# Optimization experiments

Measured on AMD Instinct MI355X. Metric: run time of the kernel, lower is better.

## Reference

```python
import jax, jax.numpy as jnp
import numpy as np

N = 50000      # nodes
E = 800000     # edges
F = 128        # input features
H = 128        # hidden dim
G = 1024       # graphs in batch
EPS = 1e-5


def setup_inputs() -> dict:
    key = jax.random.key(0)
    ks = jax.random.split(key, 16)
    s = 0.05
    return {
        "x": jax.random.normal(ks[0], (N, F), dtype=jnp.float32),
        "edge_index": jax.random.randint(ks[1], (2, E), 0, N, dtype=jnp.int64),
        "batch": jnp.sort(jax.random.randint(ks[2], (N,), 0, G, dtype=jnp.int64)),
        "convW0": jax.random.normal(ks[3], (F, H), dtype=jnp.float32) * s,
        "convW": jax.random.normal(ks[4], (2, H, H), dtype=jnp.float32) * s,  # layers 1,2
        "convb": jax.random.normal(ks[5], (3, H), dtype=jnp.float32) * s,
        "bn_gamma": jnp.ones((3, H), dtype=jnp.float32),
        "bn_beta": jnp.zeros((3, H), dtype=jnp.float32),
        "mW1": jax.random.normal(ks[6], (2 * H, 256), dtype=jnp.float32) * s,
        "mb1": jnp.zeros((256,), dtype=jnp.float32),
        "mW2": jax.random.normal(ks[7], (256, 128), dtype=jnp.float32) * s,
        "mb2": jnp.zeros((128,), dtype=jnp.float32),
        "mW3": jax.random.normal(ks[8], (128, 1), dtype=jnp.float32) * s,
        "mb3": jnp.zeros((1,), dtype=jnp.float32),
    }


def _gcn_norm(edge_index):
    # add self-loops, compute sym-normalization coeffs (PyG GCNConv default)
    loop = jnp.arange(N, dtype=edge_index.dtype)
    src = jnp.concatenate([edge_index[0], loop])
    dst = jnp.concatenate([edge_index[1], loop])
    deg = jax.ops.segment_sum(jnp.ones_like(dst, dtype=jnp.float32), dst, num_segments=N)
    dinv = jax.lax.rsqrt(deg)  # deg >= 1 due to self loops
    norm = dinv[src] * dinv[dst]  # [E+N]
    return src, dst, norm


def _gcn_layer(x, W, b, src, dst, norm):
    h = x @ W                               # [N, H]
    msg = h[src] * norm[:, None]            # gather + scale, [E+N, H]
    agg = jax.ops.segment_sum(msg, dst, num_segments=N)
    return agg + b


def _batchnorm(x, gamma, beta):
    mu = jnp.mean(x, axis=0)
    var = jnp.mean(jnp.square(x - mu), axis=0)  # biased, as torch training fwd
    return gamma * (x - mu) * jax.lax.rsqrt(var + EPS) + beta


def reference(x, edge_index, batch, convW0, convW, convb, bn_gamma, bn_beta,
              mW1, mb1, mW2, mb2, mW3, mb3):
    src, dst, norm = _gcn_norm(edge_index)
    Ws = [convW0, convW[0], convW[1]]
    for i in range(3):
        x = _gcn_layer(x, Ws[i], convb[i], src, dst, norm)
        x = _batchnorm(x, bn_gamma[i], bn_beta[i])
        x = jax.nn.relu(x)
        # dropout: identity in eval mode
    ones = jnp.ones((N,), dtype=x.dtype)
    counts = jax.ops.segment_sum(ones, batch, num_segments=G)  # [G]
    x_mean = jax.ops.segment_sum(x, batch, num_segments=G) / jnp.maximum(counts, 1.0)[:, None]
    x_max = jax.ops.segment_max(x, batch, num_segments=G)
    x_max = jnp.where(counts[:, None] > 0, x_max, 0.0)
    g = jnp.concatenate([x_mean, x_max], axis=1)  # [G, 2H]
    h = jax.nn.relu(g @ mW1 + mb1)
    h = jax.nn.relu(h @ mW2 + mb2)
    out = h @ mW3 + mb3                            # [G, 1]
    return out.squeeze(1)
```

## Files before the change

kernel.cpp:

```cpp
#include <hip/hip_runtime.h>


constexpr int FH = 128;
constexpr int GG = 1024;
constexpr int NSB = 256;
constexpr int BKS = 1024;
constexpr int CPAD = 16;
constexpr int EPB = 4096;
constexpr float EPSV = 1e-5f;

typedef __attribute__((ext_vector_type(8))) short short8v;
typedef __attribute__((ext_vector_type(4))) float f32x4;

__device__ inline unsigned short bf16_rn(float x) {
    unsigned u = __float_as_uint(x);
    unsigned r = (u + 0x7FFFu + ((u >> 16) & 1u)) >> 16;
    return (unsigned short)r;
}
__device__ inline float bflo(unsigned u) { return __uint_as_float(u << 16); }
__device__ inline float bfhi(unsigned u) { return __uint_as_float(u & 0xFFFF0000u); }
__device__ inline float4 bf4tof(ushort4 h) {
    return make_float4(__uint_as_float((unsigned)h.x << 16),
                       __uint_as_float((unsigned)h.y << 16),
                       __uint_as_float((unsigned)h.z << 16),
                       __uint_as_float((unsigned)h.w << 16));
}

__global__ void k_deg(const int* __restrict__ dst, unsigned* __restrict__ deg, int E) {
    int e = blockIdx.x * 256 + threadIdx.x;
    if (e < E) atomicAdd(&deg[dst[e]], 1u);
}

__global__ void k_dinv(const unsigned* __restrict__ deg, float* __restrict__ dinv, int n) {
    int i = blockIdx.x * 256 + threadIdx.x;
    if (i < n) dinv[i] = rsqrtf((float)deg[i] + 1.0f);
}

__global__ __launch_bounds__(1024) void k_scan1(const unsigned* __restrict__ deg,
                                                int* __restrict__ rowptr, int* __restrict__ bsum, int n) {
    __shared__ int wsum[16];
    int i = blockIdx.x * 1024 + threadIdx.x;
    int lane = threadIdx.x & 63, wid = threadIdx.x >> 6;
    int v = (i < n) ? (int)deg[i] : 0;
    int incl = v;
    #pragma unroll
    for (int off = 1; off < 64; off <<= 1) {
        int t = __shfl_up(incl, off, 64);
        if (lane >= off) incl += t;
    }
    if (lane == 63) wsum[wid] = incl;
    __syncthreads();
    int woff = 0;
    #pragma unroll
    for (int w = 0; w < 16; ++w) woff += (w < wid) ? wsum[w] : 0;
    if (i < n) rowptr[i] = woff + incl - v;
    if (threadIdx.x == 1023) bsum[blockIdx.x] = woff + incl;
}

__global__ void k_scan2(int* __restrict__ bsum, int* __restrict__ rowptr_n, int nb) {
    int lane = threadIdx.x;
    int v = (lane < nb) ? bsum[lane] : 0;
    int incl = v;
    #pragma unroll
    for (int off = 1; off < 64; off <<= 1) {
        int t = __shfl_up(incl, off, 64);
        if (lane >= off) incl += t;
    }
    if (lane < nb) bsum[lane] = incl - v;
    if (lane == 63) *rowptr_n = incl;
}

__global__ __launch_bounds__(1024) void k_scan3(int* __restrict__ rowptr,
                                                const int* __restrict__ bsum, int n) {
    int i = blockIdx.x * 1024 + threadIdx.x;
    if (i < n) rowptr[i] += bsum[blockIdx.x];
}

__global__ void k_bcur(const int* __restrict__ rowptr, int* __restrict__ bcur, int nbk) {
    int k = blockIdx.x * 256 + threadIdx.x;
    if (k < nbk) bcur[k * CPAD] = rowptr[k << 6];
}

__global__ __launch_bounds__(256) void k_binscatter(const int* __restrict__ src, const int* __restrict__ dst,
                                                    int* __restrict__ bcur, uint2* __restrict__ tmp,
                                                    int E, int nbk) {
    __shared__ int hist[BKS];
    int tid = threadIdx.x;
    for (int b = tid; b < nbk; b += 256) hist[b] = 0;
    __syncthreads();
    int e0 = blockIdx.x * EPB;
    int s[16], d[16];
    #pragma unroll
    for (int i = 0; i < 16; ++i) {
        int e = e0 + i * 256 + tid;
        if (e < E) {
            s[i] = src[e]; d[i] = dst[e];
            atomicAdd(&hist[d[i] >> 6], 1);
        } else d[i] = -1;
    }
    __syncthreads();
    for (int b = tid; b < nbk; b += 256) {
        int c = hist[b];
        hist[b] = c ? atomicAdd(&bcur[b * CPAD], c) : 0;
    }
    __syncthreads();
    #pragma unroll
    for (int i = 0; i < 16; ++i) {
        if (d[i] >= 0) {
            int p = atomicAdd(&hist[d[i] >> 6], 1);
            tmp[p] = make_uint2((unsigned)s[i], (unsigned)d[i]);
        }
    }
}

__global__ __launch_bounds__(256) void k_finesort(const uint2* __restrict__ tmp,
                                                  const int* __restrict__ rowptr,
                                                  int* __restrict__ csr_src, int n) {
    __shared__ int cur[64];
    int nb0 = blockIdx.x << 6;
    int tid = threadIdx.x;
    int hi = min(nb0 + 64, n);
    if (tid < 64 && nb0 + tid < n) cur[tid] = rowptr[nb0 + tid];
    __syncthreads();
    int estart = rowptr[nb0], eend = rowptr[hi];
    for (int e = estart + tid; e < eend; e += 256) {
        uint2 pr = tmp[e];
        int p = atomicAdd(&cur[pr.y & 63], 1);
        csr_src[p] = (int)pr.x;
    }
}

__global__ void k_gptr(const int* __restrict__ batch, int* __restrict__ gptr, int n) {
    int g = blockIdx.x * 256 + threadIdx.x;
    if (g > GG) return;
    int lo = 0, hi = n;
    while (lo < hi) { int mid = (lo + hi) >> 1; if (batch[mid] < g) lo = mid + 1; else hi = mid; }
    gptr[g] = lo;
}

__global__ void k_wprep(const float* __restrict__ W0, const float* __restrict__ W12,
                        unsigned short* __restrict__ Wt) {
    int t = blockIdx.x * 256 + threadIdx.x;
    int l = t >> 14, o = t & 16383;
    const float* W = (l == 0) ? W0 : W12 + (size_t)(l - 1) * 16384;
    int j = o & 7, c = (o >> 3) & 15, hi = (o >> 7) & 3, kb = (o >> 9) & 3, nt = o >> 11;
    int k = kb * 32 + hi * 8 + j;
    int col = nt * 16 + c;
    Wt[t] = bf16_rn(W[k * 128 + col]);
}

template<bool BF16IN>
__global__ __launch_bounds__(256) void k_gemm(const void* __restrict__ Xp,
                                              const unsigned short* __restrict__ Wt,
                                              const float* __restrict__ dinv,
                                              const float* __restrict__ sc,
                                              const float* __restrict__ sh,
                                              unsigned short* __restrict__ H, int n) {
    int wave = threadIdx.x >> 6, L = threadIdx.x & 63;
    int hi = L >> 4, c16 = L & 15;
    int m0 = blockIdx.x * 64 + wave * 16;
    int arow = m0 + c16;
    bool okA = arow < n;

    short8v aF[4];
    #pragma unroll
    for (int kb = 0; kb < 4; ++kb) {
        int kc = kb * 32 + hi * 8;
        float v[8];
        #pragma unroll
        for (int j = 0; j < 8; ++j) v[j] = 0.f;
        if (okA) {
            if constexpr (BF16IN) {
                const unsigned short* Xb = (const unsigned short*)Xp;
                uint4 raw = *(const uint4*)&Xb[(size_t)arow * 128 + kc];
                v[0] = bflo(raw.x); v[1] = bfhi(raw.x);
                v[2] = bflo(raw.y); v[3] = bfhi(raw.y);
                v[4] = bflo(raw.z); v[5] = bfhi(raw.z);
                v[6] = bflo(raw.w); v[7] = bfhi(raw.w);
                float4 s0 = *(const float4*)&sc[kc], s1 = *(const float4*)&sc[kc + 4];
                float4 h0 = *(const float4*)&sh[kc], h1 = *(const float4*)&sh[kc + 4];
                v[0] = fmaxf(fmaf(v[0], s0.x, h0.x), 0.f);
                v[1] = fmaxf(fmaf(v[1], s0.y, h0.y), 0.f);
                v[2] = fmaxf(fmaf(v[2], s0.z, h0.z), 0.f);
                v[3] = fmaxf(fmaf(v[3], s0.w, h0.w), 0.f);
                v[4] = fmaxf(fmaf(v[4], s1.x, h1.x), 0.f);
                v[5] = fmaxf(fmaf(v[5], s1.y, h1.y), 0.f);
                v[6] = fmaxf(fmaf(v[6], s1.z, h1.z), 0.f);
                v[7] = fmaxf(fmaf(v[7], s1.w, h1.w), 0.f);
            } else {
                const float* Xf = (const float*)Xp;
                float4 v0 = *(const float4*)&Xf[(size_t)arow * 128 + kc];
                float4 v1 = *(const float4*)&Xf[(size_t)arow * 128 + kc + 4];
                v[0] = v0.x; v[1] = v0.y; v[2] = v0.z; v[3] = v0.w;
                v[4] = v1.x; v[5] = v1.y; v[6] = v1.z; v[7] = v1.w;
            }
        }
        short8v a;
        #pragma unroll
        for (int j = 0; j < 8; ++j) a[j] = (short)bf16_rn(v[j]);
        aF[kb] = a;
    }

    f32x4 acc[8];
    #pragma unroll
    for (int nt = 0; nt < 8; ++nt) {
        acc[nt][0] = 0.f; acc[nt][1] = 0.f; acc[nt][2] = 0.f; acc[nt][3] = 0.f;
    }
    #pragma unroll
    for (int nt = 0; nt < 8; ++nt) {
        #pragma unroll
        for (int kb = 0; kb < 4; ++kb) {
            short8v bF = *(const short8v*)&Wt[(size_t)(nt * 4 + kb) * 512 + L * 8];
            acc[nt] = __builtin_amdgcn_mfma_f32_16x16x32_bf16(aF[kb], bF, acc[nt], 0, 0, 0);
        }
    }

    #pragma unroll
    for (int reg = 0; reg < 4; ++reg) {
        int row = m0 + hi * 4 + reg;
        if (row < n) {
            float dv = dinv[row];
            #pragma unroll
            for (int nt = 0; nt < 8; ++nt)
                H[(size_t)row * 128 + nt * 16 + c16] = bf16_rn(acc[nt][reg] * dv);
        }
    }
}

__global__ __launch_bounds__(256) void k_aggregate(const int* __restrict__ rowptr, const int* __restrict__ csr_src,
                                                   const float* __restrict__ dinv,
                                                   const unsigned short* __restrict__ H2,
                                                   unsigned short* __restrict__ Bo, int n) {
    int node = blockIdx.x * 8 + (threadIdx.x >> 5);
    if (node >= n) return;
    int lane = threadIdx.x & 31;
    int beg = rowptr[node], end = rowptr[node + 1];
    float dv = dinv[node];
    const ushort4* Hv = (const ushort4*)H2;
    float4 acc = bf4tof(Hv[(size_t)node * 32 + lane]);
    float4 acc2 = make_float4(0.f, 0.f, 0.f, 0.f);
    int e = beg;
    for (; e + 1 < end; e += 2) {
        int s0 = csr_src[e], s1 = csr_src[e + 1];
        float4 h0 = bf4tof(Hv[(size_t)s0 * 32 + lane]);
        float4 h1 = bf4tof(Hv[(size_t)s1 * 32 + lane]);
        acc.x += h0.x;  acc.y += h0.y;  acc.z += h0.z;  acc.w += h0.w;
        acc2.x += h1.x; acc2.y += h1.y; acc2.z += h1.z; acc2.w += h1.w;
    }
    if (e < end) {
        int s0 = csr_src[e];
        float4 h0 = bf4tof(Hv[(size_t)s0 * 32 + lane]);
        acc.x += h0.x; acc.y += h0.y; acc.z += h0.z; acc.w += h0.w;
    }
    ushort4 o;
    o.x = bf16_rn((acc.x + acc2.x) * dv);
    o.y = bf16_rn((acc.y + acc2.y) * dv);
    o.z = bf16_rn((acc.z + acc2.z) * dv);
    o.w = bf16_rn((acc.w + acc2.w) * dv);
    *(ushort4*)&Bo[(size_t)node * 128 + lane * 4] = o;
}

__global__ __launch_bounds__(256) void k_stats(const unsigned short* __restrict__ X,
                                               float* __restrict__ partials, int n) {
    __shared__ float sb[4][128];
    int tid = threadIdx.x;
    int fp = tid & 63, sub = tid >> 6;
    float s0 = 0.f, s1 = 0.f, q0 = 0.f, q1 = 0.f;
    for (int r = blockIdx.x * 4 + sub; r < n; r += NSB * 4) {
        unsigned u = *(const unsigned*)&X[(size_t)r * 128 + fp * 2];
        float v0 = bflo(u), v1 = bfhi(u);
        s0 += v0; q0 = fmaf(v0, v0, q0);
        s1 += v1; q1 = fmaf(v1, v1, q1);
    }
    sb[sub][fp * 2] = s0; sb[sub][fp * 2 + 1] = s1;
    __syncthreads();
    if (tid < 128) partials[(size_t)blockIdx.x * 256 + tid] =
        sb[0][tid] + sb[1][tid] + sb[2][tid] + sb[3][tid];
    __syncthreads();
    sb[sub][fp * 2] = q0; sb[sub][fp * 2 + 1] = q1;
    __syncthreads();
    if (tid < 128) partials[(size_t)blockIdx.x * 256 + 128 + tid] =
        sb[0][tid] + sb[1][tid] + sb[2][tid] + sb[3][tid];
}

__global__ __launch_bounds__(128) void k_finstats(const float* __restrict__ partials,
                                                  const float* __restrict__ gamma, const float* __restrict__ beta,
                                                  float* __restrict__ sc, float* __restrict__ sh, int n) {
    int f = threadIdx.x;
    float s = 0.f, q = 0.f;
    for (int b = 0; b < NSB; ++b) {
        s += partials[(size_t)b * 256 + f];
        q += partials[(size_t)b * 256 + 128 + f];
    }
    float invN = 1.0f / (float)n;
    float mu = s * invN;
    float var = fmaf(-mu, mu, q * invN);
    float scale = gamma[f] * rsqrtf(var + EPSV);
    sc[f] = scale;
    sh[f] = fmaf(-mu, scale, beta[f]);
}

__global__ __launch_bounds__(256) void k_pool(const unsigned short* __restrict__ X, const int* __restrict__ gptr,
                                              const float* __restrict__ sc, const float* __restrict__ sh,
                                              float* __restrict__ pooled) {
    __shared__ float shm[256];
    int g = blockIdx.x;
    int t = threadIdx.x;
    int f = t & 127, sub = t >> 7;
    int beg = gptr[g], end = gptr[g + 1];
    float scf = sc[f], shf = sh[f];
    float s = 0.f, m = 0.f;
    for (int r = beg + sub; r < end; r += 2) {
        float xv = __uint_as_float((unsigned)X[(size_t)r * 128 + f] << 16);
        float v = fmaxf(fmaf(xv, scf, shf), 0.f);
        s += v; m = fmaxf(m, v);
    }
    shm[t] = s;
    __syncthreads();
    if (sub == 0) {
        int c = end - beg;
        float inv = (c > 0) ? 1.0f / (float)c : 0.f;
        pooled[(size_t)g * 256 + f] = (s + shm[t + 128]) * inv;
    }
    __syncthreads();
    shm[t] = m;
    __syncthreads();
    if (sub == 1) {
        pooled[(size_t)g * 256 + 128 + f] = fmaxf(m, shm[t - 128]);
    }
}

__global__ __launch_bounds__(256) void k_mlp1(const float* __restrict__ pooled, const float* __restrict__ W1,
                                              const float* __restrict__ b1, float* __restrict__ H1) {
    __shared__ float grow[256];
    int gi = blockIdx.x, t = threadIdx.x;
    grow[t] = pooled[(size_t)gi * 256 + t];
    __syncthreads();
    float acc = b1[t];
    #pragma unroll 8
    for (int k = 0; k < 256; ++k) acc = fmaf(grow[k], W1[k * 256 + t], acc);
    H1[gi * 256 + t] = fmaxf(acc, 0.f);
}

__global__ __launch_bounds__(128) void k_mlp2(const float* __restrict__ H1, const float* __restrict__ W2,
                                              const float* __restrict__ b2, float* __restrict__ H2) {
    __shared__ float row[256];
    int gi = blockIdx.x, t = threadIdx.x;
    row[t] = H1[gi * 256 + t];
    row[t + 128] = H1[gi * 256 + t + 128];
    __syncthreads();
    float acc = b2[t];
    #pragma unroll 8
    for (int k = 0; k < 256; ++k) acc = fmaf(row[k], W2[k * 128 + t], acc);
    H2[gi * 128 + t] = fmaxf(acc, 0.f);
}

__global__ __launch_bounds__(256) void k_mlp3(const float* __restrict__ H2, const float* __restrict__ W3,
                                              const float* __restrict__ b3, float* __restrict__ out) {
    int gi = blockIdx.x * 4 + (threadIdx.x >> 6);
    int lane = threadIdx.x & 63;
    float v = H2[gi * 128 + lane] * W3[lane] + H2[gi * 128 + 64 + lane] * W3[64 + lane];
    #pragma unroll
    for (int off = 32; off; off >>= 1) v += __shfl_down(v, off);
    if (lane == 0) out[gi] = v + b3[0];
}

extern "C" void kernel_launch(void* const* d_in, const int* in_sizes, int n_in,
                              void* d_out, int out_size, void* d_ws, size_t ws_size,
                              hipStream_t stream) {
    const float* x      = (const float*)d_in[0];
    const int*   ei     = (const int*)d_in[1];
    const int*   batch  = (const int*)d_in[2];
    const float* convW0 = (const float*)d_in[3];
    const float* convW  = (const float*)d_in[4];
    const float* gamma  = (const float*)d_in[6];
    const float* beta   = (const float*)d_in[7];
    const float* mW1    = (const float*)d_in[8];
    const float* mb1    = (const float*)d_in[9];
    const float* mW2    = (const float*)d_in[10];
    const float* mb2    = (const float*)d_in[11];
    const float* mW3    = (const float*)d_in[12];
    const float* mb3    = (const float*)d_in[13];
    float* out = (float*)d_out;

    const int E = in_sizes[1] / 2;
    const int n = in_sizes[0] / FH;
    const int npad = (n + 4) & ~3;
    const int nb = (n + 1023) / 1024;
    const int nbk = (n + 63) >> 6;

    float*          A     = (float*)d_ws;
    unsigned short* H2b   = (unsigned short*)A;
    uint2*          tmp   = (uint2*)A;
    float*    B       = A + (size_t)n * FH;
    unsigned short* Bb = (unsigned short*)B;
    int*      bcur    = (int*)B;
    float*    dinv    = B + (size_t)n * FH;
    unsigned* deg     = (unsigned*)(dinv + n);
    float*    parts   = (float*)(deg + n);
    float*    sc      = parts + (size_t)NSB * 256;
    float*    sh      = sc + 128;
    float*    pooled  = sh + 128;
    float*    h1      = pooled + (size_t)GG * 256;
    float*    h2      = h1 + (size_t)GG * 256;
    int*      gptr    = (int*)(h2 + (size_t)GG * FH);
    int*      rowptr  = gptr + ((GG + 4) & ~3);
    int*      bsum    = rowptr + npad;
    int*      csrsrc  = bsum + 64;
    unsigned short* Wt = (unsigned short*)(csrsrc + ((E + 3) & ~3));

    const int* srcI = ei;
    const int* dstI = ei + E;

    hipMemsetAsync(deg, 0, (size_t)n * sizeof(unsigned), stream);
    k_deg<<<(E + 255) / 256, 256, 0, stream>>>(dstI, deg, E);
    k_dinv<<<(n + 255) / 256, 256, 0, stream>>>(deg, dinv, n);
    k_scan1<<<nb, 1024, 0, stream>>>(deg, rowptr, bsum, n);
    k_scan2<<<1, 64, 0, stream>>>(bsum, rowptr + n, nb);
    k_scan3<<<nb, 1024, 0, stream>>>(rowptr, bsum, n);
    k_bcur<<<(nbk + 255) / 256, 256, 0, stream>>>(rowptr, bcur, nbk);
    k_binscatter<<<(E + EPB - 1) / EPB, 256, 0, stream>>>(srcI, dstI, bcur, tmp, E, nbk);
    k_finesort<<<nbk, 256, 0, stream>>>(tmp, rowptr, csrsrc, n);
    k_gptr<<<(GG + 1 + 255) / 256, 256, 0, stream>>>(batch, gptr, n);
    k_wprep<<<3 * 16384 / 256, 256, 0, stream>>>(convW0, convW, Wt);

    for (int l = 0; l < 3; ++l) {
        if (l == 0)
            k_gemm<false><<<(n + 63) / 64, 256, 0, stream>>>(x, Wt, dinv, nullptr, nullptr, H2b, n);
        else
            k_gemm<true><<<(n + 63) / 64, 256, 0, stream>>>(Bb, Wt + (size_t)l * 16384, dinv, sc, sh, H2b, n);
        k_aggregate<<<(n + 7) / 8, 256, 0, stream>>>(rowptr, csrsrc, dinv, H2b, Bb, n);
        k_stats<<<NSB, 256, 0, stream>>>(Bb, parts, n);
        k_finstats<<<1, 128, 0, stream>>>(parts, gamma + l * FH, beta + l * FH, sc, sh, n);
    }

    k_pool<<<GG, 256, 0, stream>>>(Bb, gptr, sc, sh, pooled);
    k_mlp1<<<GG, 256, 0, stream>>>(pooled, mW1, mb1, h1);
    k_mlp2<<<GG, 128, 0, stream>>>(h1, mW2, mb2, h2);
    k_mlp3<<<GG / 4, 256, 0, stream>>>(h2, mW3, mb3, out);
}
```

Baseline: 421.8 us.

## Fuse setup and MLP kernels, widen aggregate loads, pack sort keys to 32 bits

Folds the dinv computation into scan1 and the bucket-cursor init into scan3, and merges mlp2 with mlp3 to cut launches and an intermediate buffer. The aggregation kernel now uses 16 lanes per node with 16-byte loads and 4-way unrolled gathers to raise memory-level parallelism. Sort temporaries are packed into a single 32-bit word, halving scatter traffic. This assumes node ids fit in 16 bits. BN statistics use fewer partial blocks, with a two-half reduction in finstats.

```diff
diff --git a/kernel.cpp b/kernel.cpp
--- a/kernel.cpp
+++ b/kernel.cpp
@@ -3,7 +3,7 @@
 
 constexpr int FH = 128;
 constexpr int GG = 1024;
-constexpr int NSB = 256;
+constexpr int NSB = 128;
 constexpr int BKS = 1024;
 constexpr int CPAD = 16;
 constexpr int EPB = 4096;
@@ -19,29 +19,20 @@
 }
 __device__ inline float bflo(unsigned u) { return __uint_as_float(u << 16); }
 __device__ inline float bfhi(unsigned u) { return __uint_as_float(u & 0xFFFF0000u); }
-__device__ inline float4 bf4tof(ushort4 h) {
-    return make_float4(__uint_as_float((unsigned)h.x << 16),
-                       __uint_as_float((unsigned)h.y << 16),
-                       __uint_as_float((unsigned)h.z << 16),
-                       __uint_as_float((unsigned)h.w << 16));
-}
 
 __global__ void k_deg(const int* __restrict__ dst, unsigned* __restrict__ deg, int E) {
     int e = blockIdx.x * 256 + threadIdx.x;
     if (e < E) atomicAdd(&deg[dst[e]], 1u);
 }
 
-__global__ void k_dinv(const unsigned* __restrict__ deg, float* __restrict__ dinv, int n) {
-    int i = blockIdx.x * 256 + threadIdx.x;
-    if (i < n) dinv[i] = rsqrtf((float)deg[i] + 1.0f);
-}
-
 __global__ __launch_bounds__(1024) void k_scan1(const unsigned* __restrict__ deg,
-                                                int* __restrict__ rowptr, int* __restrict__ bsum, int n) {
+                                                int* __restrict__ rowptr, int* __restrict__ bsum,
+                                                float* __restrict__ dinv, int n) {
     __shared__ int wsum[16];
     int i = blockIdx.x * 1024 + threadIdx.x;
     int lane = threadIdx.x & 63, wid = threadIdx.x >> 6;
     int v = (i < n) ? (int)deg[i] : 0;
+    if (i < n) dinv[i] = rsqrtf((float)v + 1.0f);
     int incl = v;
     #pragma unroll
     for (int off = 1; off < 64; off <<= 1) {
@@ -71,18 +62,18 @@
 }
 
 __global__ __launch_bounds__(1024) void k_scan3(int* __restrict__ rowptr,
-                                                const int* __restrict__ bsum, int n) {
+                                                const int* __restrict__ bsum,
+                                                int* __restrict__ bcur, int n) {
     int i = blockIdx.x * 1024 + threadIdx.x;
-    if (i < n) rowptr[i] += bsum[blockIdx.x];
-}
-
-__global__ void k_bcur(const int* __restrict__ rowptr, int* __restrict__ bcur, int nbk) {
-    int k = blockIdx.x * 256 + threadIdx.x;
-    if (k < nbk) bcur[k * CPAD] = rowptr[k << 6];
+    if (i < n) {
+        int r = rowptr[i] + bsum[blockIdx.x];
+        rowptr[i] = r;
+        if ((i & 63) == 0) bcur[(i >> 6) * CPAD] = r;
+    }
 }
 
 __global__ __launch_bounds__(256) void k_binscatter(const int* __restrict__ src, const int* __restrict__ dst,
-                                                    int* __restrict__ bcur, uint2* __restrict__ tmp,
+                                                    int* __restrict__ bcur, unsigned* __restrict__ tmp,
                                                     int E, int nbk) {
     __shared__ int hist[BKS];
     int tid = threadIdx.x;
@@ -108,12 +99,12 @@
     for (int i = 0; i < 16; ++i) {
         if (d[i] >= 0) {
             int p = atomicAdd(&hist[d[i] >> 6], 1);
-            tmp[p] = make_uint2((unsigned)s[i], (unsigned)d[i]);
+            tmp[p] = (unsigned)s[i] | ((unsigned)(d[i] & 63) << 16);
         }
     }
 }
 
-__global__ __launch_bounds__(256) void k_finesort(const uint2* __restrict__ tmp,
+__global__ __launch_bounds__(256) void k_finesort(const unsigned* __restrict__ tmp,
                                                   const int* __restrict__ rowptr,
                                                   int* __restrict__ csr_src, int n) {
     __shared__ int cur[64];
@@ -124,9 +115,9 @@
     __syncthreads();
     int estart = rowptr[nb0], eend = rowptr[hi];
     for (int e = estart + tid; e < eend; e += 256) {
-        uint2 pr = tmp[e];
-        int p = atomicAdd(&cur[pr.y & 63], 1);
-        csr_src[p] = (int)pr.x;
+        unsigned pr = tmp[e];
+        int p = atomicAdd(&cur[(pr >> 16) & 63], 1);
+        csr_src[p] = (int)(pr & 0xFFFFu);
     }
 }
 
@@ -231,33 +222,47 @@
                                                    const float* __restrict__ dinv,
                                                    const unsigned short* __restrict__ H2,
                                                    unsigned short* __restrict__ Bo, int n) {
-    int node = blockIdx.x * 8 + (threadIdx.x >> 5);
+    int node = blockIdx.x * 16 + (threadIdx.x >> 4);
     if (node >= n) return;
-    int lane = threadIdx.x & 31;
+    int lane = threadIdx.x & 15;
     int beg = rowptr[node], end = rowptr[node + 1];
     float dv = dinv[node];
-    const ushort4* Hv = (const ushort4*)H2;
-    float4 acc = bf4tof(Hv[(size_t)node * 32 + lane]);
-    float4 acc2 = make_float4(0.f, 0.f, 0.f, 0.f);
+    const uint4* Hv = (const uint4*)H2;
+    float a0[8], a1[8];
+    {
+        uint4 u = Hv[(size_t)node * 16 + lane];
+        a0[0] = bflo(u.x); a0[1] = bfhi(u.x); a0[2] = bflo(u.y); a0[3] = bfhi(u.y);
+        a0[4] = bflo(u.z); a0[5] = bfhi(u.z); a0[6] = bflo(u.w); a0[7] = bfhi(u.w);
+        #pragma unroll
+        for (int j = 0; j < 8; ++j) a1[j] = 0.f;
+    }
     int e = beg;
-    for (; e + 1 < end; e += 2) {
-        int s0 = csr_src[e], s1 = csr_src[e + 1];
-        float4 h0 = bf4tof(Hv[(size_t)s0 * 32 + lane]);
-        float4 h1 = bf4tof(Hv[(size_t)s1 * 32 + lane]);
-        acc.x += h0.x;  acc.y += h0.y;  acc.z += h0.z;  acc.w += h0.w;
-        acc2.x += h1.x; acc2.y += h1.y; acc2.z += h1.z; acc2.w += h1.w;
-    }
-    if (e < end) {
+    for (; e + 3 < end; e += 4) {
+        int s0 = csr_src[e], s1 = csr_src[e + 1], s2 = csr_src[e + 2], s3 = csr_src[e + 3];
+        uint4 u0 = Hv[(size_t)s0 * 16 + lane];
+        uint4 u1 = Hv[(size_t)s1 * 16 + lane];
+        uint4 u2 = Hv[(size_t)s2 * 16 + lane];
+        uint4 u3 = Hv[(size_t)s3 * 16 + lane];
+        a0[0] += bflo(u0.x); a0[1] += bfhi(u0.x); a0[2] += bflo(u0.y); a0[3] += bfhi(u0.y);
+        a0[4] += bflo(u0.z); a0[5] += bfhi(u0.z); a0[6] += bflo(u0.w); a0[7] += bfhi(u0.w);
+        a1[0] += bflo(u1.x); a1[1] += bfhi(u1.x); a1[2] += bflo(u1.y); a1[3] += bfhi(u1.y);
+        a1[4] += bflo(u1.z); a1[5] += bfhi(u1.z); a1[6] += bflo(u1.w); a1[7] += bfhi(u1.w);
+        a0[0] += bflo(u2.x); a0[1] += bfhi(u2.x); a0[2] += bflo(u2.y); a0[3] += bfhi(u2.y);
+        a0[4] += bflo(u2.z); a0[5] += bfhi(u2.z); a0[6] += bflo(u2.w); a0[7] += bfhi(u2.w);
+        a1[0] += bflo(u3.x); a1[1] += bfhi(u3.x); a1[2] += bflo(u3.y); a1[3] += bfhi(u3.y);
+        a1[4] += bflo(u3.z); a1[5] += bfhi(u3.z); a1[6] += bflo(u3.w); a1[7] += bfhi(u3.w);
+    }
+    for (; e < end; ++e) {
         int s0 = csr_src[e];
-        float4 h0 = bf4tof(Hv[(size_t)s0 * 32 + lane]);
-        acc.x += h0.x; acc.y += h0.y; acc.z += h0.z; acc.w += h0.w;
-    }
-    ushort4 o;
-    o.x = bf16_rn((acc.x + acc2.x) * dv);
-    o.y = bf16_rn((acc.y + acc2.y) * dv);
-    o.z = bf16_rn((acc.z + acc2.z) * dv);
-    o.w = bf16_rn((acc.w + acc2.w) * dv);
-    *(ushort4*)&Bo[(size_t)node * 128 + lane * 4] = o;
+        uint4 u0 = Hv[(size_t)s0 * 16 + lane];
+        a0[0] += bflo(u0.x); a0[1] += bfhi(u0.x); a0[2] += bflo(u0.y); a0[3] += bfhi(u0.y);
+        a0[4] += bflo(u0.z); a0[5] += bfhi(u0.z); a0[6] += bflo(u0.w); a0[7] += bfhi(u0.w);
+    }
+    unsigned w0 = (unsigned)bf16_rn((a0[0] + a1[0]) * dv) | ((unsigned)bf16_rn((a0[1] + a1[1]) * dv) << 16);
+    unsigned w1 = (unsigned)bf16_rn((a0[2] + a1[2]) * dv) | ((unsigned)bf16_rn((a0[3] + a1[3]) * dv) << 16);
+    unsigned w2 = (unsigned)bf16_rn((a0[4] + a1[4]) * dv) | ((unsigned)bf16_rn((a0[5] + a1[5]) * dv) << 16);
+    unsigned w3 = (unsigned)bf16_rn((a0[6] + a1[6]) * dv) | ((unsigned)bf16_rn((a0[7] + a1[7]) * dv) << 16);
+    ((uint4*)Bo)[(size_t)node * 16 + lane] = make_uint4(w0, w1, w2, w3);
 }
 
 __global__ __launch_bounds__(256) void k_stats(const unsigned short* __restrict__ X,
@@ -283,21 +288,32 @@
         sb[0][tid] + sb[1][tid] + sb[2][tid] + sb[3][tid];
 }
 
-__global__ __launch_bounds__(128) void k_finstats(const float* __restrict__ partials,
+__global__ __launch_bounds__(256) void k_finstats(const float* __restrict__ partials,
                                                   const float* __restrict__ gamma, const float* __restrict__ beta,
                                                   float* __restrict__ sc, float* __restrict__ sh, int n) {
-    int f = threadIdx.x;
+    __shared__ float red[256];
+    int t = threadIdx.x;
+    int f = t & 127, half = t >> 7;
     float s = 0.f, q = 0.f;
-    for (int b = 0; b < NSB; ++b) {
+    for (int b = half * (NSB / 2); b < (half + 1) * (NSB / 2); ++b) {
         s += partials[(size_t)b * 256 + f];
         q += partials[(size_t)b * 256 + 128 + f];
     }
-    float invN = 1.0f / (float)n;
-    float mu = s * invN;
-    float var = fmaf(-mu, mu, q * invN);
-    float scale = gamma[f] * rsqrtf(var + EPSV);
-    sc[f] = scale;
-    sh[f] = fmaf(-mu, scale, beta[f]);
+    red[t] = s;
+    __syncthreads();
+    float s_tot = red[f] + red[f + 128];
+    __syncthreads();
+    red[t] = q;
+    __syncthreads();
+    if (half == 0) {
+        float q_tot = red[f] + red[f + 128];
+        float invN = 1.0f / (float)n;
+        float mu = s_tot * invN;
+        float var = fmaf(-mu, mu, q_tot * invN);
+        float scale = gamma[f] * rsqrtf(var + EPSV);
+        sc[f] = scale;
+        sh[f] = fmaf(-mu, scale, beta[f]);
+    }
 }
 
 __global__ __launch_bounds__(256) void k_pool(const unsigned short* __restrict__ X, const int* __restrict__ gptr,
@@ -342,9 +358,11 @@
     H1[gi * 256 + t] = fmaxf(acc, 0.f);
 }
 
-__global__ __launch_bounds__(128) void k_mlp2(const float* __restrict__ H1, const float* __restrict__ W2,
-                                              const float* __restrict__ b2, float* __restrict__ H2) {
+__global__ __launch_bounds__(128) void k_mlp23(const float* __restrict__ H1, const float* __restrict__ W2,
+                                               const float* __restrict__ b2, const float* __restrict__ W3,
+                                               const float* __restrict__ b3, float* __restrict__ out) {
     __shared__ float row[256];
+    __shared__ float wred[2];
     int gi = blockIdx.x, t = threadIdx.x;
     row[t] = H1[gi * 256 + t];
     row[t + 128] = H1[gi * 256 + t + 128];
@@ -352,17 +370,12 @@
     float acc = b2[t];
     #pragma unroll 8
     for (int k = 0; k < 256; ++k) acc = fmaf(row[k], W2[k * 128 + t], acc);
-    H2[gi * 128 + t] = fmaxf(acc, 0.f);
-}
-
-__global__ __launch_bounds__(256) void k_mlp3(const float* __restrict__ H2, const float* __restrict__ W3,
-                                              const float* __restrict__ b3, float* __restrict__ out) {
-    int gi = blockIdx.x * 4 + (threadIdx.x >> 6);
-    int lane = threadIdx.x & 63;
-    float v = H2[gi * 128 + lane] * W3[lane] + H2[gi * 128 + 64 + lane] * W3[64 + lane];
+    float v = fmaxf(acc, 0.f) * W3[t];
     #pragma unroll
     for (int off = 32; off; off >>= 1) v += __shfl_down(v, off);
-    if (lane == 0) out[gi] = v + b3[0];
+    if ((t & 63) == 0) wred[t >> 6] = v;
+    __syncthreads();
+    if (t == 0) out[gi] = wred[0] + wred[1] + b3[0];
 }
 
 extern "C" void kernel_launch(void* const* d_in, const int* in_sizes, int n_in,
@@ -391,7 +404,7 @@
 
     float*          A     = (float*)d_ws;
     unsigned short* H2b   = (unsigned short*)A;
-    uint2*          tmp   = (uint2*)A;
+    unsigned*       tmp   = (unsigned*)A;
     float*    B       = A + (size_t)n * FH;
     unsigned short* Bb = (unsigned short*)B;
     int*      bcur    = (int*)B;
@@ -402,8 +415,7 @@
     float*    sh      = sc + 128;
     float*    pooled  = sh + 128;
     float*    h1      = pooled + (size_t)GG * 256;
-    float*    h2      = h1 + (size_t)GG * 256;
-    int*      gptr    = (int*)(h2 + (size_t)GG * FH);
+    int*      gptr    = (int*)(h1 + (size_t)GG * 256);
     int*      rowptr  = gptr + ((GG + 4) & ~3);
     int*      bsum    = rowptr + npad;
     int*      csrsrc  = bsum + 64;
@@ -414,11 +426,9 @@
 
     hipMemsetAsync(deg, 0, (size_t)n * sizeof(unsigned), stream);
     k_deg<<<(E + 255) / 256, 256, 0, stream>>>(dstI, deg, E);
-    k_dinv<<<(n + 255) / 256, 256, 0, stream>>>(deg, dinv, n);
-    k_scan1<<<nb, 1024, 0, stream>>>(deg, rowptr, bsum, n);
+    k_scan1<<<nb, 1024, 0, stream>>>(deg, rowptr, bsum, dinv, n);
     k_scan2<<<1, 64, 0, stream>>>(bsum, rowptr + n, nb);
-    k_scan3<<<nb, 1024, 0, stream>>>(rowptr, bsum, n);
-    k_bcur<<<(nbk + 255) / 256, 256, 0, stream>>>(rowptr, bcur, nbk);
+    k_scan3<<<nb, 1024, 0, stream>>>(rowptr, bsum, bcur, n);
     k_binscatter<<<(E + EPB - 1) / EPB, 256, 0, stream>>>(srcI, dstI, bcur, tmp, E, nbk);
     k_finesort<<<nbk, 256, 0, stream>>>(tmp, rowptr, csrsrc, n);
     k_gptr<<<(GG + 1 + 255) / 256, 256, 0, stream>>>(batch, gptr, n);
@@ -429,13 +439,12 @@
             k_gemm<false><<<(n + 63) / 64, 256, 0, stream>>>(x, Wt, dinv, nullptr, nullptr, H2b, n);
         else
             k_gemm<true><<<(n + 63) / 64, 256, 0, stream>>>(Bb, Wt + (size_t)l * 16384, dinv, sc, sh, H2b, n);
-        k_aggregate<<<(n + 7) / 8, 256, 0, stream>>>(rowptr, csrsrc, dinv, H2b, Bb, n);
+        k_aggregate<<<(n + 15) / 16, 256, 0, stream>>>(rowptr, csrsrc, dinv, H2b, Bb, n);
         k_stats<<<NSB, 256, 0, stream>>>(Bb, parts, n);
-        k_finstats<<<1, 128, 0, stream>>>(parts, gamma + l * FH, beta + l * FH, sc, sh, n);
+        k_finstats<<<1, 256, 0, stream>>>(parts, gamma + l * FH, beta + l * FH, sc, sh, n);
     }
 
     k_pool<<<GG, 256, 0, stream>>>(Bb, gptr, sc, sh, pooled);
     k_mlp1<<<GG, 256, 0, stream>>>(pooled, mW1, mb1, h1);
-    k_mlp2<<<GG, 128, 0, stream>>>(h1, mW2, mb2, h2);
-    k_mlp3<<<GG / 4, 256, 0, stream>>>(h2, mW3, mb3, out);
-}
+    k_mlp23<<<GG, 128, 0, stream>>>(h1, mW2, mb2, mW3, mb3, out);
+}
```

Result: slower. 459.1 us (+8.9%).
